# Kernel tuning notes

Hardware: AMD Instinct MI355X
Metric: run time of the kernel (lower is better)

Reference implementation:

```python
import jax, jax.numpy as jnp
import numpy as np

D_MODEL = 1024
NUM_HEADS = 16
HEAD_DIM = D_MODEL // NUM_HEADS  # 64
D_FF = 4096
EPS = 1e-5


def layer_norm(x, gamma, beta):
    mu = jnp.mean(x, axis=-1, keepdims=True)
    var = jnp.mean((x - mu) ** 2, axis=-1, keepdims=True)
    return (x - mu) * jax.lax.rsqrt(var + EPS) * gamma + beta


def apply_rope(t):
    # t: [B, H, S, head_dim]; interleaved-pair rotation as in RoPE.apply_rope
    S, d = t.shape[-2], t.shape[-1]
    inv_freq = 1.0 / (10000.0 ** (jnp.arange(0, d, 2, dtype=jnp.float32) / d))  # [d/2]
    angles = jnp.arange(S, dtype=jnp.float32)[:, None] * inv_freq[None, :]      # [S, d/2]
    sin, cos = jnp.sin(angles), jnp.cos(angles)
    tp = t.reshape(*t.shape[:-1], d // 2, 2)  # pairs of adjacent elements
    t0, t1 = tp[..., 0], tp[..., 1]
    rot = jnp.stack([t0 * cos - t1 * sin, t0 * sin + t1 * cos], axis=-1)
    return rot.reshape(t.shape)


def setup_inputs() -> dict:
    key = jax.random.key(0)
    ks = jax.random.split(key, 18)
    s = 0.02
    d, f = D_MODEL, D_FF
    return {
        "x": jax.random.normal(ks[0], (2, 2048, d), dtype=jnp.float32),
        "Wq": jax.random.normal(ks[1], (d, d), dtype=jnp.float32) * s,
        "bq": jnp.zeros((d,), jnp.float32),
        "Wk": jax.random.normal(ks[2], (d, d), dtype=jnp.float32) * s,
        "bk": jnp.zeros((d,), jnp.float32),
        "Wv": jax.random.normal(ks[3], (d, d), dtype=jnp.float32) * s,
        "bv": jnp.zeros((d,), jnp.float32),
        "Wo": jax.random.normal(ks[4], (d, d), dtype=jnp.float32) * s,
        "bo": jnp.zeros((d,), jnp.float32),
        "W1": jax.random.normal(ks[5], (d, f), dtype=jnp.float32) * s,
        "b1": jnp.zeros((f,), jnp.float32),
        "W2": jax.random.normal(ks[6], (f, d), dtype=jnp.float32) * s,
        "b2": jnp.zeros((d,), jnp.float32),
        "g1": jnp.ones((d,), jnp.float32),
        "beta1": jnp.zeros((d,), jnp.float32),
        "g2": jnp.ones((d,), jnp.float32),
        "beta2": jnp.zeros((d,), jnp.float32),
    }


def reference(x, Wq, bq, Wk, bk, Wv, bv, Wo, bo, W1, b1, W2, b2, g1, beta1, g2, beta2):
    B, S, d = x.shape
    H, hd = NUM_HEADS, HEAD_DIM
    x_norm = layer_norm(x, g1, beta1)
    q = (x_norm @ Wq + bq).reshape(B, S, H, hd).transpose(0, 2, 1, 3)  # [B,H,S,hd]
    k = (x_norm @ Wk + bk).reshape(B, S, H, hd).transpose(0, 2, 1, 3)
    v = (x_norm @ Wv + bv).reshape(B, S, H, hd).transpose(0, 2, 1, 3)
    q = apply_rope(q)
    k = apply_rope(k)
    q = q * (1.0 / jnp.sqrt(jnp.float32(hd)))
    scores = jnp.einsum("bhqd,bhkd->bhqk", q, k)  # [B,H,S,S]
    attn = jax.nn.softmax(scores, axis=-1)
    out = jnp.einsum("bhqk,bhkd->bhqd", attn, v)
    out = out.transpose(0, 2, 1, 3).reshape(B, S, d)
    attn_out = out @ Wo + bo
    x = x + attn_out  # dropout p=0 (eval)
    x_norm2 = layer_norm(x, g2, beta2)
    ffn = jax.nn.relu(x_norm2 @ W1 + b1) @ W2 + b2
    return x + ffn
```

## Files before the change

kernel.cpp:

```cpp
#include <hip/hip_runtime.h>

typedef unsigned short bf16_t;
typedef short short8 __attribute__((ext_vector_type(8)));
typedef float f32x4 __attribute__((ext_vector_type(4)));
typedef float f32x16 __attribute__((ext_vector_type(16)));
typedef unsigned int u32x4 __attribute__((ext_vector_type(4)));

static __device__ __forceinline__ unsigned short f2bf(float f) {
  unsigned int u = __float_as_uint(f);
  unsigned int r = (u + 0x7FFFu + ((u >> 16) & 1u)) >> 16;
  return (unsigned short)r;
}
static __device__ __forceinline__ float bf2f(unsigned short u) {
  return __uint_as_float((unsigned int)u << 16);
}
static __device__ __forceinline__ unsigned int cvt_pk_bf16(float lo, float hi) {
  unsigned int r;
  asm("v_cvt_pk_bf16_f32 %0, %1, %2" : "=v"(r) : "v"(lo), "v"(hi));
  return r;
}
static __device__ __forceinline__ void pl32swap(unsigned int& a, unsigned int& b) {
  asm("v_permlane32_swap_b32 %0, %1" : "+v"(a), "+v"(b));
}

__device__ __forceinline__ void gload_lds16(const void* g, void* l) {
  __builtin_amdgcn_global_load_lds((const __attribute__((address_space(1))) void*)g,
                                   (__attribute__((address_space(3))) void*)l,
                                   16, 0, 0);
}

__global__ __launch_bounds__(256) void prep_kernel(
    const float* __restrict__ Wq, const float* __restrict__ Wk,
    const float* __restrict__ Wv, const float* __restrict__ Wo,
    const float* __restrict__ W1, const float* __restrict__ W2,
    const float* __restrict__ x, const float* __restrict__ g1,
    const float* __restrict__ be1,
    bf16_t* __restrict__ WqkvT, bf16_t* __restrict__ W1T,
    bf16_t* __restrict__ W2T, bf16_t* __restrict__ xnb) {
  __shared__ float tile[32][33];
  const int bid = blockIdx.x;
  if (bid < 12288) {
    const float* src;
    bf16_t* dst;
    int rows, cols, bx, by;
    if (bid < 4096) {
      const int z = bid >> 10, r = bid & 1023;
      src = (z == 0) ? Wq : (z == 1) ? Wk : (z == 2) ? Wv : Wo;
      dst = WqkvT + (size_t)z * 1048576;
      rows = 1024; cols = 1024;
      bx = (r & 31) * 32; by = (r >> 5) * 32;
    } else if (bid < 8192) {
      const int r = bid - 4096;
      src = W1; dst = W1T; rows = 1024; cols = 4096;
      bx = (r & 127) * 32; by = (r >> 7) * 32;
    } else {
      const int r = bid - 8192;
      src = W2; dst = W2T; rows = 4096; cols = 1024;
      bx = (r & 31) * 32; by = (r >> 5) * 32;
    }
    const int tx = threadIdx.x & 31, ty = threadIdx.x >> 5;
#pragma unroll
    for (int i = 0; i < 32; i += 8)
      tile[ty + i][tx] = src[(size_t)(by + ty + i) * cols + (bx + tx)];
    __syncthreads();
#pragma unroll
    for (int i = 0; i < 32; i += 8)
      dst[(size_t)(bx + ty + i) * rows + (by + tx)] = f2bf(tile[tx][ty + i]);
  } else {
    const int row = bid - 12288;
    const int tid = threadIdx.x;
    const float4 v = reinterpret_cast<const float4*>(x + (size_t)row * 1024)[tid];
    float s = v.x + v.y + v.z + v.w;
    float ss = v.x * v.x + v.y * v.y + v.z * v.z + v.w * v.w;
#pragma unroll
    for (int off = 32; off; off >>= 1) {
      s += __shfl_xor(s, off, 64);
      ss += __shfl_xor(ss, off, 64);
    }
    float* red = &tile[0][0];
    const int wave = tid >> 6, lane = tid & 63;
    if (lane == 0) { red[wave] = s; red[4 + wave] = ss; }
    __syncthreads();
    const float mu = (red[0] + red[1] + red[2] + red[3]) * (1.f / 1024.f);
    const float ms = (red[4] + red[5] + red[6] + red[7]) * (1.f / 1024.f);
    const float rstd = rsqrtf(ms - mu * mu + 1e-5f);
    const float4 gg = reinterpret_cast<const float4*>(g1)[tid];
    const float4 bb = reinterpret_cast<const float4*>(be1)[tid];
    bf16_t* o = xnb + (size_t)row * 1024 + tid * 4;
    o[0] = f2bf((v.x - mu) * rstd * gg.x + bb.x);
    o[1] = f2bf((v.y - mu) * rstd * gg.y + bb.y);
    o[2] = f2bf((v.z - mu) * rstd * gg.z + bb.z);
    o[3] = f2bf((v.w - mu) * rstd * gg.w + bb.w);
  }
}

__global__ __launch_bounds__(256) void ln2_combine(const bf16_t* __restrict__ p,
                                                   const float* __restrict__ x,
                                                   const float* __restrict__ bo,
                                                   const float* __restrict__ g,
                                                   const float* __restrict__ be,
                                                   float* __restrict__ x2,
                                                   bf16_t* __restrict__ xn) {
  const int row = blockIdx.x;
  const int tid = threadIdx.x;
  const float4 xv = reinterpret_cast<const float4*>(x + (size_t)row * 1024)[tid];
  const float4 bb = reinterpret_cast<const float4*>(bo)[tid];
  float4 v = {bb.x + xv.x, bb.y + xv.y, bb.z + xv.z, bb.w + xv.w};
#pragma unroll
  for (int z = 0; z < 4; ++z) {
    const ushort4 a = reinterpret_cast<const ushort4*>(p + (size_t)z * 4194304 + (size_t)row * 1024)[tid];
    v.x += bf2f(a.x); v.y += bf2f(a.y); v.z += bf2f(a.z); v.w += bf2f(a.w);
  }
  reinterpret_cast<float4*>(x2 + (size_t)row * 1024)[tid] = v;
  float s = v.x + v.y + v.z + v.w;
  float ss = v.x * v.x + v.y * v.y + v.z * v.z + v.w * v.w;
#pragma unroll
  for (int off = 32; off; off >>= 1) {
    s += __shfl_xor(s, off, 64);
    ss += __shfl_xor(ss, off, 64);
  }
  __shared__ float red[8];
  const int wave = tid >> 6, lane = tid & 63;
  if (lane == 0) { red[wave] = s; red[4 + wave] = ss; }
  __syncthreads();
  const float mu = (red[0] + red[1] + red[2] + red[3]) * (1.f / 1024.f);
  const float ms = (red[4] + red[5] + red[6] + red[7]) * (1.f / 1024.f);
  const float rstd = rsqrtf(ms - mu * mu + 1e-5f);
  const float4 gg = reinterpret_cast<const float4*>(g)[tid];
  const float4 eb = reinterpret_cast<const float4*>(be)[tid];
  bf16_t* o = xn + (size_t)row * 1024 + tid * 4;
  o[0] = f2bf((v.x - mu) * rstd * gg.x + eb.x);
  o[1] = f2bf((v.y - mu) * rstd * gg.y + eb.y);
  o[2] = f2bf((v.z - mu) * rstd * gg.z + eb.z);
  o[3] = f2bf((v.w - mu) * rstd * gg.w + eb.w);
}

__global__ __launch_bounds__(256) void ffn_combine(const bf16_t* __restrict__ p0,
                                                   const bf16_t* __restrict__ p2,
                                                   const float* __restrict__ x2,
                                                   const float* __restrict__ b2,
                                                   float* __restrict__ out) {
  const int row = blockIdx.x;
  const int tid = threadIdx.x;
  const ushort4 a0 = reinterpret_cast<const ushort4*>(p0 + (size_t)row * 1024)[tid];
  const ushort4 a1 = reinterpret_cast<const ushort4*>(p0 + 4194304 + (size_t)row * 1024)[tid];
  const ushort4 a2 = reinterpret_cast<const ushort4*>(p2 + (size_t)row * 1024)[tid];
  const float4 xv = reinterpret_cast<const float4*>(x2 + (size_t)row * 1024)[tid];
  const float4 bb = reinterpret_cast<const float4*>(b2)[tid];
  float4 v;
  v.x = bf2f(a0.x) + bf2f(a1.x) + bf2f(a2.x) + bb.x + xv.x;
  v.y = bf2f(a0.y) + bf2f(a1.y) + bf2f(a2.y) + bb.y + xv.y;
  v.z = bf2f(a0.z) + bf2f(a1.z) + bf2f(a2.z) + bb.z + xv.z;
  v.w = bf2f(a0.w) + bf2f(a1.w) + bf2f(a2.w) + bb.w + xv.w;
  reinterpret_cast<float4*>(out + (size_t)row * 1024)[tid] = v;
}

__global__ __launch_bounds__(256) void rope_bf16(bf16_t* __restrict__ q,
                                                 bf16_t* __restrict__ k) {
  const int id = blockIdx.x * 256 + threadIdx.x;
  const int i = id & 31;
  const int s = (id >> 5) & 2047;
  const int bh = id >> 16;
  const float inv = exp2f((float)i * -0.41524101186f);
  float sn, cs;
  sincosf((float)s * inv, &sn, &cs);
  const size_t base = ((size_t)bh * 2048 + s) * 64 + 2 * i;
  unsigned int qp = *(unsigned int*)&q[base];
  unsigned int kp = *(unsigned int*)&k[base];
  const float q0 = bf2f(qp & 0xffff), q1 = bf2f(qp >> 16);
  const float k0 = bf2f(kp & 0xffff), k1 = bf2f(kp >> 16);
  const float qs = 0.18033688f;
  const unsigned int qo =
      (unsigned int)f2bf((q0 * cs - q1 * sn) * qs) |
      ((unsigned int)f2bf((q0 * sn + q1 * cs) * qs) << 16);
  const unsigned int ko =
      (unsigned int)f2bf(k0 * cs - k1 * sn) |
      ((unsigned int)f2bf(k0 * sn + k1 * cs) << 16);
  *(unsigned int*)&q[base] = qo;
  *(unsigned int*)&k[base] = ko;
}

__global__ __launch_bounds__(256) void vtrans(const bf16_t* __restrict__ v,
                                              bf16_t* __restrict__ vt) {
  __shared__ bf16_t tile[32][33];
  const int bh = blockIdx.x;
  const int s0 = blockIdx.y * 32;
  const int d0 = blockIdx.z * 32;
  const int tx = threadIdx.x & 31, ty = threadIdx.x >> 5;
  const size_t base = (size_t)bh * (2048 * 64);
#pragma unroll
  for (int i = 0; i < 32; i += 8)
    tile[ty + i][tx] = v[base + (size_t)(s0 + ty + i) * 64 + d0 + tx];
  __syncthreads();
#pragma unroll
  for (int i = 0; i < 32; i += 8)
    vt[base + (size_t)(d0 + ty + i) * 2048 + s0 + tx] = tile[tx][ty + i];
}

__global__ __launch_bounds__(256, 2) void attn5(const bf16_t* __restrict__ qb,
                                                const bf16_t* __restrict__ kb,
                                                const bf16_t* __restrict__ vt,
                                                bf16_t* __restrict__ out) {
  const int bh = blockIdx.x;
  const int tid = threadIdx.x, wave = tid >> 6, lane = tid & 63;
  const int l31 = lane & 31, hi = lane >> 5;
  const int q0 = blockIdx.y * 128 + wave * 32;
  const size_t kvb = (size_t)bh * (2048 * 64);

  __shared__ __align__(16) bf16_t Ks[2][4096];
  __shared__ __align__(16) bf16_t Vs[2][4096];

  short8 qf[4];
#pragma unroll
  for (int st = 0; st < 4; ++st)
    qf[st] = *(const short8*)&qb[kvb + (size_t)(q0 + l31) * 64 + st * 16 + hi * 8];

  int kidx[2][4];
  int vidx[2][2][2];
#pragma unroll
  for (int st = 0; st < 4; ++st) {
    const int R0 = l31, R1 = 32 + l31;
    kidx[0][st] = (R0 * 8 + (((st << 1) | hi) ^ (R0 & 7))) * 8;
    kidx[1][st] = (R1 * 8 + (((st << 1) | hi) ^ (R1 & 7))) * 8;
  }
#pragma unroll
  for (int f = 0; f < 2; ++f)
#pragma unroll
    for (int ks = 0; ks < 2; ++ks) {
      const int R0 = l31, R1 = 32 + l31;
      vidx[0][f][ks] = (R0 * 8 + (((f << 2) | (ks << 1) | hi) ^ (R0 & 7))) * 8;
      vidx[1][f][ks] = (R1 * 8 + (((f << 2) | (ks << 1) | hi) ^ (R1 & 7))) * 8;
    }

  short8 vones;
#pragma unroll
  for (int j = 0; j < 8; ++j) vones[j] = (short)0x3F80;

  f32x16 acc0 = {}, acc1 = {}, lacc = {};
  const f32x16 fz = {};

#pragma unroll
  for (int j = 0; j < 2; ++j) {
    const int s = wave * 128 + j * 64 + lane;
    const int r = s >> 3;
    const int c = (s & 7) ^ (r & 7);
    gload_lds16(kb + kvb + (size_t)r * 64 + c * 8, &Ks[0][(size_t)s * 8]);
    gload_lds16(vt + kvb + (size_t)r * 2048 + c * 8, &Vs[0][(size_t)s * 8]);
  }
  __syncthreads();

#define ATTN_TILE(BUF, TPREF, DOPREF)                                                     \
  {                                                                                       \
    if (DOPREF) {                                                                         \
      _Pragma("unroll") for (int j = 0; j < 2; ++j) {                                     \
        const int s = wave * 128 + j * 64 + lane;                                         \
        const int r = s >> 3;                                                             \
        const int c = (s & 7) ^ (r & 7);                                                  \
        gload_lds16(kb + kvb + (size_t)((TPREF) + r) * 64 + c * 8,                        \
                    &Ks[(BUF) ^ 1][(size_t)s * 8]);                                       \
        gload_lds16(vt + kvb + (size_t)r * 2048 + (TPREF) + c * 8,                        \
                    &Vs[(BUF) ^ 1][(size_t)s * 8]);                                       \
      }                                                                                   \
    }                                                                                     \
    short8 kfa[4], kfb[4];                                                                \
    _Pragma("unroll") for (int st = 0; st < 4; ++st) {                                    \
      kfa[st] = *(const short8*)&Ks[BUF][kidx[0][st]];                                    \
      kfb[st] = *(const short8*)&Ks[BUF][kidx[1][st]];                                    \
    }                                                                                     \
    __builtin_amdgcn_s_setprio(1);                                                        \
    f32x16 p0 = __builtin_amdgcn_mfma_f32_32x32x16_bf16(kfa[0], qf[0], fz, 0, 0, 0);      \
    f32x16 p1 = __builtin_amdgcn_mfma_f32_32x32x16_bf16(kfb[0], qf[0], fz, 0, 0, 0);      \
    _Pragma("unroll") for (int st = 1; st < 4; ++st) {                                    \
      p0 = __builtin_amdgcn_mfma_f32_32x32x16_bf16(kfa[st], qf[st], p0, 0, 0, 0);         \
      p1 = __builtin_amdgcn_mfma_f32_32x32x16_bf16(kfb[st], qf[st], p1, 0, 0, 0);         \
    }                                                                                     \
    __builtin_amdgcn_s_setprio(0);                                                        \
    _Pragma("unroll") for (int f = 0; f < 2; ++f) {                                       \
      f32x16& p = f ? p1 : p0;                                                            \
      float e[16];                                                                        \
      _Pragma("unroll") for (int r = 0; r < 16; ++r) e[r] = exp2f(p[r]);                  \
      unsigned int a0 = cvt_pk_bf16(e[0], e[1]), b0 = cvt_pk_bf16(e[4], e[5]);            \
      unsigned int a1 = cvt_pk_bf16(e[2], e[3]), b1 = cvt_pk_bf16(e[6], e[7]);            \
      unsigned int a2 = cvt_pk_bf16(e[8], e[9]), b2 = cvt_pk_bf16(e[12], e[13]);          \
      unsigned int a3 = cvt_pk_bf16(e[10], e[11]), b3 = cvt_pk_bf16(e[14], e[15]);        \
      pl32swap(a0, b0);                                                                   \
      pl32swap(a1, b1);                                                                   \
      pl32swap(a2, b2);                                                                   \
      pl32swap(a3, b3);                                                                   \
      const u32x4 w0 = {a0, a1, b0, b1};                                                  \
      const u32x4 w1 = {a2, a3, b2, b3};                                                  \
      const short8 pf0 = __builtin_bit_cast(short8, w0);                                  \
      const short8 pf1 = __builtin_bit_cast(short8, w1);                                  \
      const short8 vf00 = *(const short8*)&Vs[BUF][vidx[0][f][0]];                        \
      const short8 vf10 = *(const short8*)&Vs[BUF][vidx[1][f][0]];                        \
      const short8 vf01 = *(const short8*)&Vs[BUF][vidx[0][f][1]];                        \
      const short8 vf11 = *(const short8*)&Vs[BUF][vidx[1][f][1]];                        \
      __builtin_amdgcn_s_setprio(1);                                                      \
      lacc = __builtin_amdgcn_mfma_f32_32x32x16_bf16(pf0, vones, lacc, 0, 0, 0);          \
      acc0 = __builtin_amdgcn_mfma_f32_32x32x16_bf16(pf0, vf00, acc0, 0, 0, 0);           \
      acc1 = __builtin_amdgcn_mfma_f32_32x32x16_bf16(pf0, vf10, acc1, 0, 0, 0);           \
      lacc = __builtin_amdgcn_mfma_f32_32x32x16_bf16(pf1, vones, lacc, 0, 0, 0);          \
      acc0 = __builtin_amdgcn_mfma_f32_32x32x16_bf16(pf1, vf01, acc0, 0, 0, 0);           \
      acc1 = __builtin_amdgcn_mfma_f32_32x32x16_bf16(pf1, vf11, acc1, 0, 0, 0);           \
      __builtin_amdgcn_s_setprio(0);                                                      \
    }                                                                                     \
    __syncthreads();                                                                      \
  }

  for (int t = 0; t < 1920; t += 128) {
    ATTN_TILE(0, t + 64, 1)
    ATTN_TILE(1, t + 128, 1)
  }
  ATTN_TILE(0, 1984, 1)
  ATTN_TILE(1, 0, 0)
#undef ATTN_TILE

  const int b = bh >> 4, h = bh & 15;
#pragma unroll
  for (int r = 0; r < 16; ++r) {
    const int qrow = (r & 3) + 8 * (r >> 2) + 4 * hi;
    const float rl = 1.f / lacc[r];
    const size_t ro = (size_t)(b * 2048 + q0 + qrow) * 1024 + h * 64;
    out[ro + l31] = f2bf(acc0[r] * rl);
    out[ro + 32 + l31] = f2bf(acc1[r] * rl);
  }
}

enum { MODE_QKV = 0, MODE_FF1 = 1, MODE_PART = 2 };

template <int MODE>
__global__ __launch_bounds__(256) void gemm_bt(
    const bf16_t* __restrict__ A, const bf16_t* __restrict__ BT,
    int M, int N, int K, int kspan,
    const float* __restrict__ bias0, const float* __restrict__ bias1,
    const float* __restrict__ bias2,
    bf16_t* __restrict__ ob0, bf16_t* __restrict__ ob1, bf16_t* __restrict__ ob2) {
  __shared__ __align__(16) char smem[34816];
  bf16_t* As = (bf16_t*)smem;
  bf16_t* Bs = (bf16_t*)(smem + 16384);
  const int tid = threadIdx.x;
  const int wave = tid >> 6, lane = tid & 63;
  const int row16 = lane & 15, quad = lane >> 4;
  const int m0 = blockIdx.x * 128, n0 = blockIdx.y * 128;
  const int wm = (wave & 1) << 6, wn = (wave >> 1) << 6;

  f32x4 acc[4][4];
#pragma unroll
  for (int i = 0; i < 4; ++i)
#pragma unroll
    for (int j = 0; j < 4; ++j) acc[i][j] = (f32x4){0.f, 0.f, 0.f, 0.f};

  const int kb = blockIdx.z * kspan;
  const int kend = (kb + kspan < K) ? kb + kspan : K;

  for (int k0 = kb; k0 < kend; k0 += 64) {
#pragma unroll
    for (int j = 0; j < 4; ++j) {
      const int s = j * 256 + tid;
      const int r = s >> 3;
      const int cg = ((s & 7) ^ (r & 7)) << 3;
      gload_lds16(A + (size_t)(m0 + r) * K + k0 + cg, As + (size_t)s * 8);
      gload_lds16(BT + (size_t)(n0 + r) * K + k0 + cg, Bs + (size_t)s * 8);
    }
    __syncthreads();
    const int sw = row16 & 7;
#pragma unroll
    for (int kk = 0; kk < 2; ++kk) {
      short8 af[4], bfr[4];
#pragma unroll
      for (int mi = 0; mi < 4; ++mi)
        af[mi] = *(const short8*)&As[(size_t)(wm + mi * 16 + row16) * 64 + (((kk << 2) | quad) ^ sw) * 8];
#pragma unroll
      for (int ni = 0; ni < 4; ++ni)
        bfr[ni] = *(const short8*)&Bs[(size_t)(wn + ni * 16 + row16) * 64 + (((kk << 2) | quad) ^ sw) * 8];
#pragma unroll
      for (int mi = 0; mi < 4; ++mi)
#pragma unroll
        for (int ni = 0; ni < 4; ++ni)
          acc[mi][ni] =
              __builtin_amdgcn_mfma_f32_16x16x32_bf16(af[mi], bfr[ni], acc[mi][ni], 0, 0, 0);
    }
    __syncthreads();
  }

  bf16_t* ct = (bf16_t*)smem;
#pragma unroll
  for (int mi = 0; mi < 4; ++mi)
#pragma unroll
    for (int ni = 0; ni < 4; ++ni) {
      const int gn = n0 + wn + ni * 16 + row16;
      float bsv = 0.f;
      if (MODE == MODE_QKV)
        bsv = (gn < 1024) ? bias0[gn] : (gn < 2048) ? bias1[gn - 1024] : bias2[gn - 2048];
      else if (MODE == MODE_FF1)
        bsv = bias0[gn];
#pragma unroll
      for (int r = 0; r < 4; ++r) {
        float c = acc[mi][ni][r] + bsv;
        if (MODE == MODE_FF1) c = fmaxf(c, 0.f);
        ct[(size_t)(wm + mi * 16 + quad * 4 + r) * 136 + wn + ni * 16 + row16] = f2bf(c);
      }
    }
  __syncthreads();
  const int lr0 = tid >> 4, lc = tid & 15;
#pragma unroll
  for (int i = 0; i < 8; ++i) {
    const int lr = i * 16 + lr0;
    const uint4 v = *(const uint4*)&ct[(size_t)lr * 136 + lc * 8];
    const int gm = m0 + lr;
    if (MODE == MODE_QKV) {
      const int nn = (n0 & 1023) + lc * 8;
      const int h = nn >> 6, d = nn & 63;
      const int b = gm >> 11, s = gm & 2047;
      bf16_t* dst = (n0 < 1024) ? ob0 : (n0 < 2048) ? ob1 : ob2;
      *(uint4*)&dst[(((size_t)b * 16 + h) * 2048 + s) * 64 + d] = v;
    } else if (MODE == MODE_FF1) {
      *(uint4*)&ob0[(size_t)gm * N + n0 + lc * 8] = v;
    } else {
      bf16_t* dst = (blockIdx.z == 2) ? ob1 : ob0 + (size_t)blockIdx.z * 4194304;
      *(uint4*)&dst[(size_t)gm * N + n0 + lc * 8] = v;
    }
  }
}

extern "C" void kernel_launch(void* const* d_in, const int* in_sizes, int n_in,
                              void* d_out, int out_size, void* d_ws, size_t ws_size,
                              hipStream_t stream) {
  const float* x = (const float*)d_in[0];
  const float* Wq = (const float*)d_in[1];
  const float* bq = (const float*)d_in[2];
  const float* Wk = (const float*)d_in[3];
  const float* bk = (const float*)d_in[4];
  const float* Wv = (const float*)d_in[5];
  const float* bv = (const float*)d_in[6];
  const float* Wo = (const float*)d_in[7];
  const float* bo = (const float*)d_in[8];
  const float* W1 = (const float*)d_in[9];
  const float* b1 = (const float*)d_in[10];
  const float* W2 = (const float*)d_in[11];
  const float* b2 = (const float*)d_in[12];
  const float* g1 = (const float*)d_in[13];
  const float* be1 = (const float*)d_in[14];
  const float* g2 = (const float*)d_in[15];
  const float* be2 = (const float*)d_in[16];
  float* out = (float*)d_out;

  char* ws = (char*)d_ws;
  size_t off = 0;
  auto alloc = [&](size_t bytes) {
    void* p = ws + off;
    off += (bytes + 255) & ~(size_t)255;
    return p;
  };
  bf16_t* WqkvT = (bf16_t*)alloc(3072ULL * 1024 * 2);
  bf16_t* WoT = (bf16_t*)alloc(1024ULL * 1024 * 2);
  bf16_t* W1T = (bf16_t*)alloc(4096ULL * 1024 * 2);
  bf16_t* W2T = (bf16_t*)alloc(1024ULL * 4096 * 2);
  bf16_t* xnb = (bf16_t*)alloc(4096ULL * 1024 * 2);
  bf16_t* qb = (bf16_t*)alloc(4194304ULL * 2);
  bf16_t* kb = (bf16_t*)alloc(4194304ULL * 2);
  bf16_t* vraw = (bf16_t*)alloc(4194304ULL * 2);
  bf16_t* vt = (bf16_t*)alloc(4194304ULL * 2);
  bf16_t* h1 = qb;
  bf16_t* x2p = qb;
  bf16_t* ffp = WqkvT;
  float* x2 = (float*)alloc(16777216ULL);

  prep_kernel<<<16384, 256, 0, stream>>>(Wq, Wk, Wv, Wo, W1, W2, x, g1, be1,
                                         WqkvT, W1T, W2T, xnb);

  gemm_bt<MODE_QKV><<<dim3(32, 24, 1), 256, 0, stream>>>(xnb, WqkvT, 4096, 3072, 1024, 1024,
                                                         bq, bk, bv, qb, kb, vraw);

  rope_bf16<<<8192, 256, 0, stream>>>(qb, kb);

  vtrans<<<dim3(32, 64, 2), 256, 0, stream>>>(vraw, vt);

  attn5<<<dim3(32, 16), 256, 0, stream>>>(qb, kb, vt, xnb);

  gemm_bt<MODE_PART><<<dim3(32, 8, 4), 256, 0, stream>>>(xnb, WoT, 4096, 1024, 1024, 256,
                                                         nullptr, nullptr, nullptr,
                                                         x2p, x2p + 2 * 4194304, nullptr);

  ln2_combine<<<4096, 256, 0, stream>>>(x2p, x, bo, g2, be2, x2, xnb);

  gemm_bt<MODE_FF1><<<dim3(32, 32, 1), 256, 0, stream>>>(xnb, W1T, 4096, 4096, 1024, 1024,
                                                         b1, nullptr, nullptr,
                                                         h1, nullptr, nullptr);

  gemm_bt<MODE_PART><<<dim3(32, 8, 3), 256, 0, stream>>>(h1, W2T, 4096, 1024, 4096, 1408,
                                                         nullptr, nullptr, nullptr,
                                                         ffp, xnb, nullptr);

  ffn_combine<<<4096, 256, 0, stream>>>(ffp, xnb, x2, b2, out);
}
```

Measured before the change: 365.3 us.

## Process 128-key tiles per iteration with partial vmcnt waits in attention

Restructures the attention main loop to stage two 64-key sub-tiles (128 keys) per double-buffered LDS slot. Both QK products are issued before the softmax/PV work, so more MFMA work can be in flight. The full __syncthreads after each tile is replaced by an explicit s_waitcnt vmcnt(8) plus s_barrier, which lets the next prefetch stay outstanding while the current tile is consumed. This halves the number of barriers per key range. In exchange, LDS use doubles to 64KB per block, which may limit the two-blocks-per-CU occupancy, and register pressure rises from the four live score accumulators.

Result: no change. 364.7 us (-0.2%).

```diff
diff --git a/kernel.cpp b/kernel.cpp
--- a/kernel.cpp
+++ b/kernel.cpp
@@ -197,7 +197,7 @@
     vt[base + (size_t)(d0 + ty + i) * 2048 + s0 + tx] = tile[tx][ty + i];
 }
 
-__global__ __launch_bounds__(256, 2) void attn5(const bf16_t* __restrict__ qb,
+__global__ __launch_bounds__(256, 2) void attn6(const bf16_t* __restrict__ qb,
                                                 const bf16_t* __restrict__ kb,
                                                 const bf16_t* __restrict__ vt,
                                                 bf16_t* __restrict__ out) {
@@ -207,8 +207,8 @@
   const int q0 = blockIdx.y * 128 + wave * 32;
   const size_t kvb = (size_t)bh * (2048 * 64);
 
-  __shared__ __align__(16) bf16_t Ks[2][4096];
-  __shared__ __align__(16) bf16_t Vs[2][4096];
+  __shared__ __align__(16) bf16_t Ks[2][2][4096];
+  __shared__ __align__(16) bf16_t Vs[2][2][4096];
 
   short8 qf[4];
 #pragma unroll
@@ -239,81 +239,103 @@
   f32x16 acc0 = {}, acc1 = {}, lacc = {};
   const f32x16 fz = {};
 
-#pragma unroll
-  for (int j = 0; j < 2; ++j) {
-    const int s = wave * 128 + j * 64 + lane;
-    const int r = s >> 3;
-    const int c = (s & 7) ^ (r & 7);
-    gload_lds16(kb + kvb + (size_t)r * 64 + c * 8, &Ks[0][(size_t)s * 8]);
-    gload_lds16(vt + kvb + (size_t)r * 2048 + c * 8, &Vs[0][(size_t)s * 8]);
-  }
-  __syncthreads();
-
-#define ATTN_TILE(BUF, TPREF, DOPREF)                                                     \
-  {                                                                                       \
-    if (DOPREF) {                                                                         \
-      _Pragma("unroll") for (int j = 0; j < 2; ++j) {                                     \
-        const int s = wave * 128 + j * 64 + lane;                                         \
-        const int r = s >> 3;                                                             \
-        const int c = (s & 7) ^ (r & 7);                                                  \
-        gload_lds16(kb + kvb + (size_t)((TPREF) + r) * 64 + c * 8,                        \
-                    &Ks[(BUF) ^ 1][(size_t)s * 8]);                                       \
-        gload_lds16(vt + kvb + (size_t)r * 2048 + (TPREF) + c * 8,                        \
-                    &Vs[(BUF) ^ 1][(size_t)s * 8]);                                       \
-      }                                                                                   \
-    }                                                                                     \
-    short8 kfa[4], kfb[4];                                                                \
-    _Pragma("unroll") for (int st = 0; st < 4; ++st) {                                    \
-      kfa[st] = *(const short8*)&Ks[BUF][kidx[0][st]];                                    \
-      kfb[st] = *(const short8*)&Ks[BUF][kidx[1][st]];                                    \
-    }                                                                                     \
-    __builtin_amdgcn_s_setprio(1);                                                        \
-    f32x16 p0 = __builtin_amdgcn_mfma_f32_32x32x16_bf16(kfa[0], qf[0], fz, 0, 0, 0);      \
-    f32x16 p1 = __builtin_amdgcn_mfma_f32_32x32x16_bf16(kfb[0], qf[0], fz, 0, 0, 0);      \
-    _Pragma("unroll") for (int st = 1; st < 4; ++st) {                                    \
-      p0 = __builtin_amdgcn_mfma_f32_32x32x16_bf16(kfa[st], qf[st], p0, 0, 0, 0);         \
-      p1 = __builtin_amdgcn_mfma_f32_32x32x16_bf16(kfb[st], qf[st], p1, 0, 0, 0);         \
-    }                                                                                     \
-    __builtin_amdgcn_s_setprio(0);                                                        \
-    _Pragma("unroll") for (int f = 0; f < 2; ++f) {                                       \
-      f32x16& p = f ? p1 : p0;                                                            \
-      float e[16];                                                                        \
-      _Pragma("unroll") for (int r = 0; r < 16; ++r) e[r] = exp2f(p[r]);                  \
-      unsigned int a0 = cvt_pk_bf16(e[0], e[1]), b0 = cvt_pk_bf16(e[4], e[5]);            \
-      unsigned int a1 = cvt_pk_bf16(e[2], e[3]), b1 = cvt_pk_bf16(e[6], e[7]);            \
-      unsigned int a2 = cvt_pk_bf16(e[8], e[9]), b2 = cvt_pk_bf16(e[12], e[13]);          \
-      unsigned int a3 = cvt_pk_bf16(e[10], e[11]), b3 = cvt_pk_bf16(e[14], e[15]);        \
-      pl32swap(a0, b0);                                                                   \
-      pl32swap(a1, b1);                                                                   \
-      pl32swap(a2, b2);                                                                   \
-      pl32swap(a3, b3);                                                                   \
-      const u32x4 w0 = {a0, a1, b0, b1};                                                  \
-      const u32x4 w1 = {a2, a3, b2, b3};                                                  \
-      const short8 pf0 = __builtin_bit_cast(short8, w0);                                  \
-      const short8 pf1 = __builtin_bit_cast(short8, w1);                                  \
-      const short8 vf00 = *(const short8*)&Vs[BUF][vidx[0][f][0]];                        \
-      const short8 vf10 = *(const short8*)&Vs[BUF][vidx[1][f][0]];                        \
-      const short8 vf01 = *(const short8*)&Vs[BUF][vidx[0][f][1]];                        \
-      const short8 vf11 = *(const short8*)&Vs[BUF][vidx[1][f][1]];                        \
-      __builtin_amdgcn_s_setprio(1);                                                      \
-      lacc = __builtin_amdgcn_mfma_f32_32x32x16_bf16(pf0, vones, lacc, 0, 0, 0);          \
-      acc0 = __builtin_amdgcn_mfma_f32_32x32x16_bf16(pf0, vf00, acc0, 0, 0, 0);           \
-      acc1 = __builtin_amdgcn_mfma_f32_32x32x16_bf16(pf0, vf10, acc1, 0, 0, 0);           \
-      lacc = __builtin_amdgcn_mfma_f32_32x32x16_bf16(pf1, vones, lacc, 0, 0, 0);          \
-      acc0 = __builtin_amdgcn_mfma_f32_32x32x16_bf16(pf1, vf01, acc0, 0, 0, 0);           \
-      acc1 = __builtin_amdgcn_mfma_f32_32x32x16_bf16(pf1, vf11, acc1, 0, 0, 0);           \
-      __builtin_amdgcn_s_setprio(0);                                                      \
-    }                                                                                     \
-    __syncthreads();                                                                      \
-  }
-
-  for (int t = 0; t < 1920; t += 128) {
-    ATTN_TILE(0, t + 64, 1)
-    ATTN_TILE(1, t + 128, 1)
-  }
-  ATTN_TILE(0, 1984, 1)
-  ATTN_TILE(1, 0, 0)
-#undef ATTN_TILE
+#define STAGE(DST, T0)                                                                     \
+  {                                                                                        \
+    _Pragma("unroll") for (int sub = 0; sub < 2; ++sub) {                                  \
+      _Pragma("unroll") for (int j = 0; j < 2; ++j) {                                      \
+        const int s = wave * 128 + j * 64 + lane;                                          \
+        const int r = s >> 3;                                                              \
+        const int c = (s & 7) ^ (r & 7);                                                   \
+        gload_lds16(kb + kvb + (size_t)((T0) + sub * 64 + r) * 64 + c * 8,                 \
+                    &Ks[DST][sub][(size_t)s * 8]);                                         \
+        gload_lds16(vt + kvb + (size_t)r * 2048 + (T0) + sub * 64 + c * 8,                 \
+                    &Vs[DST][sub][(size_t)s * 8]);                                         \
+      }                                                                                    \
+    }                                                                                      \
+  }
+
+#define QK(BUF, SUB, P0, P1)                                                               \
+  {                                                                                        \
+    short8 kfa[4], kfb[4];                                                                 \
+    _Pragma("unroll") for (int st = 0; st < 4; ++st) {                                     \
+      kfa[st] = *(const short8*)&Ks[BUF][SUB][kidx[0][st]];                                \
+      kfb[st] = *(const short8*)&Ks[BUF][SUB][kidx[1][st]];                                \
+    }                                                                                      \
+    __builtin_amdgcn_s_setprio(1);                                                         \
+    P0 = __builtin_amdgcn_mfma_f32_32x32x16_bf16(kfa[0], qf[0], fz, 0, 0, 0);              \
+    P1 = __builtin_amdgcn_mfma_f32_32x32x16_bf16(kfb[0], qf[0], fz, 0, 0, 0);              \
+    _Pragma("unroll") for (int st = 1; st < 4; ++st) {                                     \
+      P0 = __builtin_amdgcn_mfma_f32_32x32x16_bf16(kfa[st], qf[st], P0, 0, 0, 0);          \
+      P1 = __builtin_amdgcn_mfma_f32_32x32x16_bf16(kfb[st], qf[st], P1, 0, 0, 0);          \
+    }                                                                                      \
+    __builtin_amdgcn_s_setprio(0);                                                         \
+  }
+
+#define SMPV(BUF, SUB, P0, P1)                                                             \
+  {                                                                                        \
+    _Pragma("unroll") for (int f = 0; f < 2; ++f) {                                        \
+      f32x16& p = f ? P1 : P0;                                                             \
+      float e[16];                                                                         \
+      _Pragma("unroll") for (int r = 0; r < 16; ++r) e[r] = exp2f(p[r]);                   \
+      unsigned int a0 = cvt_pk_bf16(e[0], e[1]), b0 = cvt_pk_bf16(e[4], e[5]);             \
+      unsigned int a1 = cvt_pk_bf16(e[2], e[3]), b1 = cvt_pk_bf16(e[6], e[7]);             \
+      unsigned int a2 = cvt_pk_bf16(e[8], e[9]), b2 = cvt_pk_bf16(e[12], e[13]);           \
+      unsigned int a3 = cvt_pk_bf16(e[10], e[11]), b3 = cvt_pk_bf16(e[14], e[15]);         \
+      pl32swap(a0, b0);                                                                    \
+      pl32swap(a1, b1);                                                                    \
+      pl32swap(a2, b2);                                                                    \
+      pl32swap(a3, b3);                                                                    \
+      const u32x4 w0 = {a0, a1, b0, b1};                                                   \
+      const u32x4 w1 = {a2, a3, b2, b3};                                                   \
+      const short8 pf0 = __builtin_bit_cast(short8, w0);                                   \
+      const short8 pf1 = __builtin_bit_cast(short8, w1);                                   \
+      const short8 vf00 = *(const short8*)&Vs[BUF][SUB][vidx[0][f][0]];                    \
+      const short8 vf10 = *(const short8*)&Vs[BUF][SUB][vidx[1][f][0]];                    \
+      const short8 vf01 = *(const short8*)&Vs[BUF][SUB][vidx[0][f][1]];                    \
+      const short8 vf11 = *(const short8*)&Vs[BUF][SUB][vidx[1][f][1]];                    \
+      __builtin_amdgcn_s_setprio(1);                                                       \
+      lacc = __builtin_amdgcn_mfma_f32_32x32x16_bf16(pf0, vones, lacc, 0, 0, 0);           \
+      acc0 = __builtin_amdgcn_mfma_f32_32x32x16_bf16(pf0, vf00, acc0, 0, 0, 0);            \
+      acc1 = __builtin_amdgcn_mfma_f32_32x32x16_bf16(pf0, vf10, acc1, 0, 0, 0);            \
+      lacc = __builtin_amdgcn_mfma_f32_32x32x16_bf16(pf1, vones, lacc, 0, 0, 0);           \
+      acc0 = __builtin_amdgcn_mfma_f32_32x32x16_bf16(pf1, vf01, acc0, 0, 0, 0);            \
+      acc1 = __builtin_amdgcn_mfma_f32_32x32x16_bf16(pf1, vf11, acc1, 0, 0, 0);            \
+      __builtin_amdgcn_s_setprio(0);                                                       \
+    }                                                                                      \
+  }
+
+#define CITER(BUF, NT0, DOPREF)                                                            \
+  {                                                                                        \
+    if (DOPREF) {                                                                          \
+      STAGE((BUF) ^ 1, NT0);                                                               \
+      asm volatile("s_waitcnt vmcnt(8)" ::: "memory");                                     \
+    } else {                                                                               \
+      asm volatile("s_waitcnt vmcnt(0)" ::: "memory");                                     \
+    }                                                                                      \
+    __builtin_amdgcn_s_barrier();                                                          \
+    asm volatile("" ::: "memory");                                                         \
+    f32x16 pa0, pa1, pb0, pb1;                                                             \
+    QK(BUF, 0, pa0, pa1);                                                                  \
+    QK(BUF, 1, pb0, pb1);                                                                  \
+    SMPV(BUF, 0, pa0, pa1);                                                                \
+    SMPV(BUF, 1, pb0, pb1);                                                                \
+    asm volatile("" ::: "memory");                                                         \
+    __builtin_amdgcn_s_barrier();                                                          \
+    asm volatile("" ::: "memory");                                                         \
+  }
+
+  STAGE(0, 0);
+
+  for (int k = 0; k < 7; ++k) {
+    CITER(0, (2 * k + 1) * 128, 1)
+    CITER(1, (2 * k + 2) * 128, 1)
+  }
+  CITER(0, 1920, 1)
+  CITER(1, 0, 0)
+#undef CITER
+#undef SMPV
+#undef QK
+#undef STAGE
 
   const int b = bh >> 4, h = bh & 15;
 #pragma unroll
@@ -476,7 +498,7 @@
 
   vtrans<<<dim3(32, 64, 2), 256, 0, stream>>>(vraw, vt);
 
-  attn5<<<dim3(32, 16), 256, 0, stream>>>(qb, kb, vt, xnb);
+  attn6<<<dim3(32, 16), 256, 0, stream>>>(qb, kb, vt, xnb);
 
   gemm_bt<MODE_PART><<<dim3(32, 8, 4), 256, 0, stream>>>(xnb, WoT, 4096, 1024, 1024, 256,
                                                          nullptr, nullptr, nullptr,
```
